# Optimization experiments

Measured on AMD Instinct MI355X. Metric: run time of the kernel, lower is better.

The kernel has to match this reference:

```python
import jax, jax.numpy as jnp
import numpy as np
from jax import lax

B, T, F = 8, 512, 128          # batch, mel time, mel freq
DM, DS, DC, EXP, NL = 384, 16, 4, 2, 12
DI = EXP * DM                   # 768 inner width
DTR = (DM + 15) // 16           # 24, mamba_ssm dt_rank='auto'
PT = PF = 16
L = (T // PT) * (F // PF)       # 256 patches
NC = 4


def setup_inputs() -> dict:
    key = jax.random.key(0)
    ks = iter(jax.random.split(key, 24))
    def n(shape, s=0.02):
        return jax.random.normal(next(ks), shape, jnp.float32) * s
    return {
        "x": jax.random.normal(next(ks), (B, T, F), jnp.float32),
        "patch_w": n((DM, PT, PF)),
        "patch_b": jnp.zeros((DM,), jnp.float32),
        "pos_embed": n((1, L, DM)),
        "ln_g": jnp.ones((NL, DM), jnp.float32),
        "ln_b": jnp.zeros((NL, DM), jnp.float32),
        "in_proj_w": n((NL, 2 * DI, DM)),
        "conv_w": n((NL, DI, DC), 0.1),
        "conv_b": jnp.zeros((NL, DI), jnp.float32),
        "x_proj_w": n((NL, DTR + 2 * DS, DI)),
        "dt_proj_w": n((NL, DI, DTR), 0.1),
        "dt_proj_b": n((NL, DI), 0.1),
        "A_log": jnp.tile(jnp.log(jnp.arange(1, DS + 1, dtype=jnp.float32))[None, None, :], (NL, DI, 1)),
        "Dskip": jnp.ones((NL, DI), jnp.float32),
        "out_proj_w": n((NL, DM, DI)),
        "fn_g": jnp.ones((DM,), jnp.float32),
        "fn_b": jnp.zeros((DM,), jnp.float32),
        "head_w": n((NC, DM)),
        "head_b": jnp.zeros((NC,), jnp.float32),
    }


def _layernorm(x, g, b):
    m = x.mean(-1, keepdims=True)
    v = jnp.var(x, axis=-1, keepdims=True)
    return (x - m) * lax.rsqrt(v + 1e-5) * g + b


def _silu(v):
    return v * jax.nn.sigmoid(v)


def _mamba_block(x, p):
    # x: [B, L, DM]; residual Mamba block (pre-LN, dropout=identity in eval)
    ln_g, ln_b, Wi, cw, cb, Wx, Wdt, bdt, A_log, Dsk, Wo = p
    res = x
    h = _layernorm(x, ln_g, ln_b)
    xz = jnp.einsum('bld,ed->ble', h, Wi)          # [B,L,2*DI]
    u, z = jnp.split(xz, 2, axis=-1)
    # causal depthwise conv1d, kernel DC (small, unrolled)
    up = jnp.pad(u, ((0, 0), (DC - 1, 0), (0, 0)))
    u = sum(up[:, k:k + L, :] * cw[:, k] for k in range(DC)) + cb
    u = _silu(u)
    proj = jnp.einsum('bld,ed->ble', u, Wx)        # [B,L,DTR+2*DS]
    dt, Bm, Cm = jnp.split(proj, [DTR, DTR + DS], axis=-1)
    delta = jax.nn.softplus(jnp.einsum('blr,dr->bld', dt, Wdt) + bdt)  # [B,L,DI]
    A = -jnp.exp(A_log)                            # [DI, DS]
    dA = jnp.exp(delta[..., None] * A)             # [B,L,DI,DS]
    dBu = (delta * u)[..., None] * Bm[:, :, None, :]

    def step(hst, inp):
        dA_t, dBu_t, C_t = inp
        hst = dA_t * hst + dBu_t                   # [B,DI,DS]
        return hst, jnp.einsum('bdn,bn->bd', hst, C_t)

    h0 = jnp.zeros((x.shape[0], DI, DS), x.dtype)
    _, ys = lax.scan(step, h0, (dA.swapaxes(0, 1), dBu.swapaxes(0, 1), Cm.swapaxes(0, 1)))
    y = ys.swapaxes(0, 1) + u * Dsk                # [B,L,DI]
    y = y * _silu(z)
    return res + jnp.einsum('bld,ed->ble', y, Wo)


def reference(x, patch_w, patch_b, pos_embed, ln_g, ln_b, in_proj_w, conv_w, conv_b,
              x_proj_w, dt_proj_w, dt_proj_b, A_log, Dskip, out_proj_w,
              fn_g, fn_b, head_w, head_b):
    Bn = x.shape[0]
    # patch embed = non-overlapping 16x16 conv == blocked reshape + einsum
    patches = x.reshape(Bn, T // PT, PT, F // PF, PF)
    tok = jnp.einsum('bhpwq,dpq->bhwd', patches, patch_w) + patch_b
    tok = tok.reshape(Bn, L, DM) + pos_embed

    def layer(carry, p):
        return _mamba_block(carry, p), None

    tok, _ = lax.scan(layer, tok, (ln_g, ln_b, in_proj_w, conv_w, conv_b,
                                   x_proj_w, dt_proj_w, dt_proj_b, A_log, Dskip, out_proj_w))
    tok = _layernorm(tok, fn_g, fn_b)
    pooled = tok.mean(axis=1)
    return pooled @ head_w.T + head_b
```

## Files before the change

### kernel.cpp

```cpp
#include <hip/hip_runtime.h>
#include <math.h>

namespace {

constexpr int kB   = 8;
constexpr int kL   = 256;
constexpr int kTok = 2048;
constexpr int kDM  = 384;
constexpr int kDI  = 768;
constexpr int kDS  = 16;
constexpr int kDTR = 24;
constexpr int kPROJ = 56;
constexpr int kNL  = 12;

constexpr int kWIN  = 2 * kDI * kDM;
constexpr int kWOUT = kDM * kDI;
constexpr int kWX   = kPROJ * kDI;
constexpr int kWTOT = kWIN + kWOUT + kWX;

typedef float f32x4 __attribute__((ext_vector_type(4)));
typedef short short8 __attribute__((ext_vector_type(8)));

__device__ __forceinline__ float softplus_f(float x) {
  return (x > 20.f) ? x : log1pf(__expf(x));
}
__device__ __forceinline__ float silu_f(float x) {
  return x / (1.f + __expf(-x));
}
__device__ __forceinline__ unsigned short f2bf(float f) {
  union { float f; unsigned u; } v; v.f = f;
  unsigned r = v.u + 0x7FFFu + ((v.u >> 16) & 1u);
  return (unsigned short)(r >> 16);
}
__device__ __forceinline__ float bf2f(unsigned short u) {
  return __uint_as_float((unsigned)u << 16);
}

__global__ __launch_bounds__(256) void patch_gemm_k(
    const float* __restrict__ x, const float* __restrict__ Bw,
    const float* __restrict__ bias, const float* __restrict__ pos,
    float* __restrict__ C) {
  __shared__ float As[16][68];
  __shared__ float Bs[16][68];
  int tid = threadIdx.x;
  int bm = blockIdx.y * 64;
  int bn = blockIdx.x * 64;
  int lr = tid >> 2;
  int lk = (tid & 3) << 2;
  int tm = (tid >> 4) << 2;
  int tn = (tid & 15) << 2;
  float acc[4][4] = {};
  for (int k0 = 0; k0 < 256; k0 += 16) {
    {
      int token = bm + lr;
      int b = token >> 8, l = token & 255;
      int h = l >> 3, w = l & 7;
      int p = k0 >> 4;
      const float* ap = x + ((size_t)(b * 512) + h * 16 + p) * 128 + w * 16 + lk;
      float4 av = *(const float4*)ap;
      As[lk + 0][lr] = av.x; As[lk + 1][lr] = av.y;
      As[lk + 2][lr] = av.z; As[lk + 3][lr] = av.w;
    }
    {
      const float* bp = Bw + (size_t)(bn + lr) * 256 + k0 + lk;
      float4 bv = *(const float4*)bp;
      Bs[lk + 0][lr] = bv.x; Bs[lk + 1][lr] = bv.y;
      Bs[lk + 2][lr] = bv.z; Bs[lk + 3][lr] = bv.w;
    }
    __syncthreads();
    #pragma unroll
    for (int k = 0; k < 16; ++k) {
      float4 a = *(const float4*)&As[k][tm];
      float4 b = *(const float4*)&Bs[k][tn];
      float av[4] = {a.x, a.y, a.z, a.w};
      float bv[4] = {b.x, b.y, b.z, b.w};
      #pragma unroll
      for (int i = 0; i < 4; ++i)
        #pragma unroll
        for (int j = 0; j < 4; ++j)
          acc[i][j] = fmaf(av[i], bv[j], acc[i][j]);
    }
    __syncthreads();
  }
  #pragma unroll
  for (int i = 0; i < 4; ++i) {
    int row = bm + tm + i;
    #pragma unroll
    for (int j = 0; j < 4; ++j) {
      int col = bn + tn + j;
      C[(size_t)row * kDM + col] =
          acc[i][j] + bias[col] + pos[(size_t)(row & 255) * kDM + col];
    }
  }
}

__global__ __launch_bounds__(384) void lnpool_k(
    const float* __restrict__ in, float* __restrict__ pooled,
    const float* __restrict__ g, const float* __restrict__ bb) {
  int t = blockIdx.x, d = threadIdx.x;
  float v = in[(size_t)t * kDM + d];
  float s = v, s2 = v * v;
  #pragma unroll
  for (int m = 32; m >= 1; m >>= 1) {
    s  += __shfl_xor(s, m);
    s2 += __shfl_xor(s2, m);
  }
  __shared__ float ps[6], ps2[6];
  if ((d & 63) == 0) { ps[d >> 6] = s; ps2[d >> 6] = s2; }
  __syncthreads();
  float S = 0.f, S2 = 0.f;
  #pragma unroll
  for (int i = 0; i < 6; ++i) { S += ps[i]; S2 += ps2[i]; }
  float mean = S * (1.f / 384.f);
  float var  = S2 * (1.f / 384.f) - mean * mean;
  float r = rsqrtf(var + 1e-5f);
  float o = (v - mean) * r * g[d] + bb[d];
  atomicAdd(&pooled[(size_t)(t >> 8) * kDM + d], o * (1.f / 256.f));
}

__global__ __launch_bounds__(256) void convert_all_k(
    const float* __restrict__ w_in, const float* __restrict__ w_out,
    const float* __restrict__ w_x, unsigned short* __restrict__ dst,
    float* __restrict__ pooled_zero) {
  int layer = blockIdx.y;
  int tid = threadIdx.x;
  if (layer == 0 && blockIdx.x == 0) {
    for (int i = tid; i < kB * kDM; i += 256) pooled_zero[i] = 0.f;
  }
  int i4 = (blockIdx.x * 256 + tid) * 4;
  if (i4 >= kWTOT) return;
  const float* src;
  int off;
  if (i4 < kWIN) { src = w_in + (size_t)layer * kWIN; off = i4; }
  else if (i4 < kWIN + kWOUT) { src = w_out + (size_t)layer * kWOUT; off = i4 - kWIN; }
  else { src = w_x + (size_t)layer * kWX; off = i4 - kWIN - kWOUT; }
  float4 v = *(const float4*)(src + off);
  unsigned short o[4] = {f2bf(v.x), f2bf(v.y), f2bf(v.z), f2bf(v.w)};
  *(uint2*)(dst + (size_t)layer * kWTOT + i4) = *(const uint2*)o;
}

__global__ __launch_bounds__(256) void inproj_ln_k(
    const float* __restrict__ tok, const unsigned short* __restrict__ Bw,
    const float* __restrict__ g, const float* __restrict__ bb,
    unsigned short* __restrict__ Cbf, float* __restrict__ proj_zero) {
  __shared__ __align__(16) unsigned short As[4][64][8];
  __shared__ __align__(16) unsigned short Bs[4][128][8];
  __shared__ float smean[64], srstd[64];
  __shared__ float sg_[kDM], sb_[kDM];
  int tid = threadIdx.x;
  int bm = blockIdx.y * 64;
  int bn = blockIdx.x * 128;
  {
    int bid = blockIdx.y * 12 + blockIdx.x;
    for (int i = bid * 256 + tid; i < kTok * kPROJ; i += 384 * 256)
      proj_zero[i] = 0.f;
  }
  for (int i = tid; i < kDM; i += 256) { sg_[i] = g[i]; sb_[i] = bb[i]; }
  {
    int r = tid >> 2, quarter = tid & 3;
    const float* rp = tok + (size_t)(bm + r) * kDM + quarter * 96;
    float s = 0.f, s2 = 0.f;
    #pragma unroll
    for (int q = 0; q < 24; ++q) {
      float4 v = ((const float4*)rp)[q];
      s  += v.x + v.y + v.z + v.w;
      s2 += v.x * v.x + v.y * v.y + v.z * v.z + v.w * v.w;
    }
    s  += __shfl_xor(s, 1);  s2 += __shfl_xor(s2, 1);
    s  += __shfl_xor(s, 2);  s2 += __shfl_xor(s2, 2);
    if (quarter == 0) {
      float mean = s * (1.f / 384.f);
      float var  = s2 * (1.f / 384.f) - mean * mean;
      smean[r] = mean;
      srstd[r] = rsqrtf(var + 1e-5f);
    }
  }
  __syncthreads();
  int wave = tid >> 6, lane = tid & 63;
  int lm = lane & 15, lq = lane >> 4;
  int wm = (wave & 1) * 32, wn = (wave >> 1) * 64;
  f32x4 acc[2][4] = {};
  for (int k0 = 0; k0 < kDM; k0 += 32) {
    int ar = tid & 63, aq = tid >> 6;
    unsigned short av[8];
    {
      float mean = smean[ar], rstd = srstd[ar];
      const float* ap = tok + (size_t)(bm + ar) * kDM + k0 + aq * 8;
      float4 v0 = ((const float4*)ap)[0];
      float4 v1 = ((const float4*)ap)[1];
      float vv[8] = {v0.x, v0.y, v0.z, v0.w, v1.x, v1.y, v1.z, v1.w};
      #pragma unroll
      for (int j = 0; j < 8; ++j) {
        int k = k0 + aq * 8 + j;
        av[j] = f2bf((vv[j] - mean) * rstd * sg_[k] + sb_[k]);
      }
    }
    int br = tid & 127, bq0 = tid >> 7, bq1 = bq0 + 2;
    uint4 b0 = *(const uint4*)(Bw + (size_t)(bn + br) * kDM + k0 + bq0 * 8);
    uint4 b1 = *(const uint4*)(Bw + (size_t)(bn + br) * kDM + k0 + bq1 * 8);
    __syncthreads();
    *(uint4*)&As[aq][ar][0]  = *(const uint4*)av;
    *(uint4*)&Bs[bq0][br][0] = b0;
    *(uint4*)&Bs[bq1][br][0] = b1;
    __syncthreads();
    short8 bfrag[4];
    #pragma unroll
    for (int ni = 0; ni < 4; ++ni)
      bfrag[ni] = *(const short8*)&Bs[lq][wn + ni * 16 + lm][0];
    #pragma unroll
    for (int mi = 0; mi < 2; ++mi) {
      short8 afrag = *(const short8*)&As[lq][wm + mi * 16 + lm][0];
      #pragma unroll
      for (int ni = 0; ni < 4; ++ni)
        acc[mi][ni] = __builtin_amdgcn_mfma_f32_16x16x32_bf16(
            afrag, bfrag[ni], acc[mi][ni], 0, 0, 0);
    }
  }
  #pragma unroll
  for (int mi = 0; mi < 2; ++mi) {
    #pragma unroll
    for (int ni = 0; ni < 4; ++ni) {
      int grow0 = bm + wm + mi * 16 + lq * 4;
      int gcol = bn + wn + ni * 16 + lm;
      #pragma unroll
      for (int r = 0; r < 4; ++r)
        Cbf[(size_t)(grow0 + r) * (2 * kDI) + gcol] = f2bf(acc[mi][ni][r]);
    }
  }
}

__global__ __launch_bounds__(256) void xproj_conv_k(
    const unsigned short* __restrict__ xz, const unsigned short* __restrict__ Bw,
    const float* __restrict__ cw, const float* __restrict__ cb,
    float* __restrict__ proj, unsigned short* __restrict__ uT_bf) {
  __shared__ __align__(16) unsigned short As[4][64][8];
  __shared__ __align__(16) unsigned short Bs[4][64][8];
  __shared__ float scw[128][4];
  __shared__ float scb[128];
  int tid = threadIdx.x;
  int bm = blockIdx.x * 64;
  int kbase = blockIdx.y * 128;
  int wave = tid >> 6, lane = tid & 63;
  int lm = lane & 15, lq = lane >> 4;
  int wm = wave * 16;
  f32x4 acc[4] = {};

  if (tid < 128) {
    *(float4*)&scw[tid][0] = *(const float4*)(cw + (size_t)(kbase + tid) * 4);
    scb[tid] = cb[kbase + tid];
  }
  __syncthreads();

  int ar = tid & 63;
  int aq = tid >> 6;
  int t = bm + ar;
  int b = t >> 8, l = t & 255;

  for (int kt = 0; kt < 4; ++kt) {
    int k0 = kbase + kt * 32;
    int dloc = kt * 32 + aq * 8;
    int dg = kbase + dloc;
    unsigned short av[8];
    {
      float vals[4][8];
      #pragma unroll
      for (int q = 0; q < 4; ++q) {
        if (l - 3 + q >= 0) {
          uint4 r = *(const uint4*)(xz + (size_t)(t - 3 + q) * (2 * kDI) + dg);
          const unsigned short* rs = (const unsigned short*)&r;
          #pragma unroll
          for (int j = 0; j < 8; ++j) vals[q][j] = bf2f(rs[j]);
        } else {
          #pragma unroll
          for (int j = 0; j < 8; ++j) vals[q][j] = 0.f;
        }
      }
      #pragma unroll
      for (int j = 0; j < 8; ++j) {
        float a = scb[dloc + j];
        a = fmaf(vals[0][j], scw[dloc + j][0], a);
        a = fmaf(vals[1][j], scw[dloc + j][1], a);
        a = fmaf(vals[2][j], scw[dloc + j][2], a);
        a = fmaf(vals[3][j], scw[dloc + j][3], a);
        unsigned short ub = f2bf(silu_f(a));
        av[j] = ub;
        uT_bf[((size_t)b * kDI + dg + j) * kL + l] = ub;
      }
    }
    int br = tid & 63, bq = tid >> 6;
    uint4 b0;
    if (br < kPROJ)
      b0 = *(const uint4*)(Bw + (size_t)br * kDI + k0 + bq * 8);
    else
      b0 = make_uint4(0u, 0u, 0u, 0u);
    __syncthreads();
    *(uint4*)&As[aq][ar][0] = *(const uint4*)av;
    *(uint4*)&Bs[bq][br][0] = b0;
    __syncthreads();
    short8 afrag = *(const short8*)&As[lq][wm + lm][0];
    #pragma unroll
    for (int ni = 0; ni < 4; ++ni) {
      short8 bfrag = *(const short8*)&Bs[lq][ni * 16 + lm][0];
      acc[ni] = __builtin_amdgcn_mfma_f32_16x16x32_bf16(
          afrag, bfrag, acc[ni], 0, 0, 0);
    }
  }

  #pragma unroll
  for (int ni = 0; ni < 4; ++ni) {
    int grow0 = bm + wm + lq * 4;
    int gcol = ni * 16 + lm;
    if (gcol < kPROJ) {
      #pragma unroll
      for (int r = 0; r < 4; ++r)
        atomicAdd(&proj[(size_t)(grow0 + r) * kPROJ + gcol], acc[ni][r]);
    }
  }
}

__global__ __launch_bounds__(256) void bgemm_out_k(
    const unsigned short* __restrict__ A, int lda,
    const unsigned short* __restrict__ B, int ldb,
    float* __restrict__ C, int ldc, int Kc) {
  __shared__ __align__(16) unsigned short As[4][128][8];
  __shared__ __align__(16) unsigned short Bs[4][128][8];
  int tid = threadIdx.x;
  int bm = blockIdx.y * 128;
  int bn = blockIdx.x * 128;
  int k_begin = blockIdx.z * Kc;
  int wave = tid >> 6, lane = tid & 63;
  int lm = lane & 15, lq = lane >> 4;
  int wm = (wave >> 1) * 64, wn = (wave & 1) * 64;
  f32x4 acc[4][4] = {};

  for (int kt = 0; kt < Kc; kt += 32) {
    int k0 = k_begin + kt;
    int ar0 = tid & 127, aq0 = tid >> 7;
    int aq1 = aq0 + 2;
    uint4 a0 = *(const uint4*)(A + (size_t)(bm + ar0) * lda + k0 + aq0 * 8);
    uint4 a1 = *(const uint4*)(A + (size_t)(bm + ar0) * lda + k0 + aq1 * 8);
    uint4 b0 = *(const uint4*)(B + (size_t)(bn + ar0) * ldb + k0 + aq0 * 8);
    uint4 b1 = *(const uint4*)(B + (size_t)(bn + ar0) * ldb + k0 + aq1 * 8);
    __syncthreads();
    *(uint4*)&As[aq0][ar0][0] = a0;
    *(uint4*)&As[aq1][ar0][0] = a1;
    *(uint4*)&Bs[aq0][ar0][0] = b0;
    *(uint4*)&Bs[aq1][ar0][0] = b1;
    __syncthreads();
    short8 bfrag[4];
    #pragma unroll
    for (int ni = 0; ni < 4; ++ni)
      bfrag[ni] = *(const short8*)&Bs[lq][wn + ni * 16 + lm][0];
    #pragma unroll
    for (int mi = 0; mi < 4; ++mi) {
      short8 afrag = *(const short8*)&As[lq][wm + mi * 16 + lm][0];
      #pragma unroll
      for (int ni = 0; ni < 4; ++ni)
        acc[mi][ni] = __builtin_amdgcn_mfma_f32_16x16x32_bf16(
            afrag, bfrag[ni], acc[mi][ni], 0, 0, 0);
    }
  }

  #pragma unroll
  for (int mi = 0; mi < 4; ++mi) {
    #pragma unroll
    for (int ni = 0; ni < 4; ++ni) {
      int grow0 = bm + wm + mi * 16 + lq * 4;
      int gcol = bn + wn + ni * 16 + lm;
      #pragma unroll
      for (int r = 0; r < 4; ++r)
        atomicAdd(&C[(size_t)(grow0 + r) * ldc + gcol], acc[mi][ni][r]);
    }
  }
}

__global__ __launch_bounds__(256) void scansplit_k(
    const float* __restrict__ proj, const unsigned short* __restrict__ uT_bf,
    const unsigned short* __restrict__ xz, const float* __restrict__ dtw,
    const float* __restrict__ dtb, const float* __restrict__ A_log,
    const float* __restrict__ Dsk, unsigned short* __restrict__ y_bf) {
  int d0 = blockIdx.x * 8;
  int b = blockIdx.y;
  int tid = threadIdx.x;
  int dsub = tid & 7;
  int nh = (tid >> 3) & 1;
  int c = tid >> 4;
  int d = d0 + dsub;
  __shared__ float sh[16][16][9];
  __shared__ float sca[16][16][9];

  float Av[8];
  {
    const float* ap = A_log + (size_t)d * kDS + nh * 8;
    #pragma unroll
    for (int q = 0; q < 2; ++q) {
      float4 v = ((const float4*)ap)[q];
      Av[q * 4 + 0] = -__expf(v.x);
      Av[q * 4 + 1] = -__expf(v.y);
      Av[q * 4 + 2] = -__expf(v.z);
      Av[q * 4 + 3] = -__expf(v.w);
    }
  }
  float bdt = dtb[d];
  float Dv = Dsk[d];

  const float* pr = proj + ((size_t)(b * kL) + c * 16) * kPROJ;

  float dtlo[8], dthi[8];
  {
    float wdt[24];
    const float* wp = dtw + (size_t)d * kDTR;
    #pragma unroll
    for (int q = 0; q < 6; ++q) {
      float4 v = ((const float4*)wp)[q];
      wdt[q * 4 + 0] = v.x; wdt[q * 4 + 1] = v.y;
      wdt[q * 4 + 2] = v.z; wdt[q * 4 + 3] = v.w;
    }
    const float* prm = pr + (size_t)(nh * 8) * kPROJ;
    float mine[8];
    #pragma unroll
    for (int i = 0; i < 8; ++i) {
      const float* p = prm + (size_t)i * kPROJ;
      float acc = bdt;
      #pragma unroll
      for (int q = 0; q < 6; ++q) {
        float4 v = ((const float4*)p)[q];
        acc = fmaf(v.x, wdt[q * 4 + 0], acc);
        acc = fmaf(v.y, wdt[q * 4 + 1], acc);
        acc = fmaf(v.z, wdt[q * 4 + 2], acc);
        acc = fmaf(v.w, wdt[q * 4 + 3], acc);
      }
      mine[i] = softplus_f(acc);
    }
    #pragma unroll
    for (int i = 0; i < 8; ++i) {
      float other = __shfl_xor(mine[i], 8);
      dtlo[i] = nh ? other : mine[i];
      dthi[i] = nh ? mine[i] : other;
    }
  }

  float u_[16];
  {
    const unsigned short* up = uT_bf + ((size_t)b * kDI + d) * kL + c * 16;
    uint4 v0 = ((const uint4*)up)[0];
    uint4 v1 = ((const uint4*)up)[1];
    const unsigned short* us = (const unsigned short*)&v0;
    #pragma unroll
    for (int i = 0; i < 8; ++i) u_[i] = bf2f(us[i]);
    us = (const unsigned short*)&v1;
    #pragma unroll
    for (int i = 0; i < 8; ++i) u_[8 + i] = bf2f(us[i]);
  }

  float h[8], ca[8];
  #pragma unroll
  for (int n = 0; n < 8; ++n) { h[n] = 0.f; ca[n] = 1.f; }
  #pragma unroll
  for (int i = 0; i < 16; ++i) {
    float dl = (i < 8) ? dtlo[i] : dthi[i - 8];
    float du = dl * u_[i];
    const float* p = pr + (size_t)i * kPROJ + 24 + nh * 8;
    float4 b0 = ((const float4*)p)[0];
    float4 b1 = ((const float4*)p)[1];
    float Bv[8] = {b0.x, b0.y, b0.z, b0.w, b1.x, b1.y, b1.z, b1.w};
    #pragma unroll
    for (int n = 0; n < 8; ++n) {
      float a = __expf(dl * Av[n]);
      h[n] = fmaf(a, h[n], du * Bv[n]);
      ca[n] *= a;
    }
  }
  {
    int nrow = nh * 8;
    #pragma unroll
    for (int q = 0; q < 8; ++q) {
      sh[c][nrow + q][dsub] = h[q];
      sca[c][nrow + q][dsub] = ca[q];
    }
  }
  __syncthreads();

  float h0[8];
  #pragma unroll
  for (int n = 0; n < 8; ++n) h0[n] = 0.f;
  {
    int nrow = nh * 8;
    for (int j = 0; j < c; ++j) {
      #pragma unroll
      for (int q = 0; q < 8; ++q)
        h0[q] = fmaf(sca[j][nrow + q][dsub], h0[q], sh[j][nrow + q][dsub]);
    }
  }

  float sg_[16];
  if (nh == 0) {
    const unsigned short* zp =
        xz + (size_t)(b * kL + c * 16) * (2 * kDI) + kDI + d;
    #pragma unroll
    for (int i = 0; i < 16; ++i)
      sg_[i] = silu_f(bf2f(zp[(size_t)i * (2 * kDI)]));
  }

  unsigned short* yp = y_bf + (size_t)(b * kL + c * 16) * kDI + d;
  #pragma unroll
  for (int i = 0; i < 16; ++i) {
    float dl = (i < 8) ? dtlo[i] : dthi[i - 8];
    float du = dl * u_[i];
    const float* p = pr + (size_t)i * kPROJ + 24 + nh * 8;
    float4 b0 = ((const float4*)p)[0];
    float4 b1 = ((const float4*)p)[1];
    float4 c0 = ((const float4*)(p + 16))[0];
    float4 c1 = ((const float4*)(p + 16))[1];
    float Bv[8] = {b0.x, b0.y, b0.z, b0.w, b1.x, b1.y, b1.z, b1.w};
    float Cv[8] = {c0.x, c0.y, c0.z, c0.w, c1.x, c1.y, c1.z, c1.w};
    float yv = 0.f;
    #pragma unroll
    for (int n = 0; n < 8; ++n) {
      float a = __expf(dl * Av[n]);
      h0[n] = fmaf(a, h0[n], du * Bv[n]);
      yv = fmaf(h0[n], Cv[n], yv);
    }
    yv += __shfl_xor(yv, 8);
    if (nh == 0) yp[(size_t)i * kDI] = f2bf((yv + u_[i] * Dv) * sg_[i]);
  }
}

__global__ __launch_bounds__(64) void head_k(
    const float* __restrict__ pooled, const float* __restrict__ hw,
    const float* __restrict__ hb, float* __restrict__ out) {
  int b = blockIdx.x >> 2, c = blockIdx.x & 3;
  int lane = threadIdx.x;
  float acc = 0.f;
  for (int dd = lane; dd < kDM; dd += 64)
    acc = fmaf(pooled[b * kDM + dd], hw[c * kDM + dd], acc);
  #pragma unroll
  for (int m = 32; m >= 1; m >>= 1) acc += __shfl_xor(acc, m);
  if (lane == 0) out[b * 4 + c] = acc + hb[c];
}

}

extern "C" void kernel_launch(void* const* d_in, const int* in_sizes, int n_in,
                              void* d_out, int out_size, void* d_ws, size_t ws_size,
                              hipStream_t stream) {
  (void)in_sizes; (void)n_in; (void)out_size; (void)ws_size;
  const float* x        = (const float*)d_in[0];
  const float* patch_w  = (const float*)d_in[1];
  const float* patch_b  = (const float*)d_in[2];
  const float* pos      = (const float*)d_in[3];
  const float* ln_g     = (const float*)d_in[4];
  const float* ln_b     = (const float*)d_in[5];
  const float* in_w     = (const float*)d_in[6];
  const float* conv_w   = (const float*)d_in[7];
  const float* conv_b   = (const float*)d_in[8];
  const float* xproj_w  = (const float*)d_in[9];
  const float* dtproj_w = (const float*)d_in[10];
  const float* dtproj_b = (const float*)d_in[11];
  const float* A_log    = (const float*)d_in[12];
  const float* Dskip    = (const float*)d_in[13];
  const float* out_w    = (const float*)d_in[14];
  const float* fn_g     = (const float*)d_in[15];
  const float* fn_b     = (const float*)d_in[16];
  const float* head_w   = (const float*)d_in[17];
  const float* head_b   = (const float*)d_in[18];
  float* out = (float*)d_out;

  float* ws = (float*)d_ws;
  float* tok    = ws; ws += kTok * kDM;
  float* proj   = ws; ws += kTok * kPROJ;
  float* pooled = ws; ws += kB * kDM;
  unsigned short* xz_bf = (unsigned short*)ws; ws += kTok * 2 * kDI / 2;
  unsigned short* uT_bf = (unsigned short*)ws; ws += kTok * kDI / 2;
  unsigned short* y_bf  = (unsigned short*)ws; ws += kTok * kDI / 2;
  unsigned short* w_bf  = (unsigned short*)ws; ws += (size_t)kNL * kWTOT / 2;

  convert_all_k<<<dim3(kWTOT / 4 / 256, kNL), 256, 0, stream>>>(
      in_w, out_w, xproj_w, w_bf, pooled);

  patch_gemm_k<<<dim3(6, 32), 256, 0, stream>>>(x, patch_w, patch_b, pos, tok);

  for (int layer = 0; layer < kNL; ++layer) {
    const unsigned short* wl = w_bf + (size_t)layer * kWTOT;
    inproj_ln_k<<<dim3(12, 32), 256, 0, stream>>>(
        tok, wl, ln_g + layer * kDM, ln_b + layer * kDM, xz_bf, proj);
    xproj_conv_k<<<dim3(32, 6), 256, 0, stream>>>(
        xz_bf, wl + kWIN + kWOUT, conv_w + layer * kDI * 4,
        conv_b + layer * kDI, proj, uT_bf);
    scansplit_k<<<dim3(kDI / 8, kB), 256, 0, stream>>>(
        proj, uT_bf, xz_bf, dtproj_w + (size_t)layer * kDI * kDTR,
        dtproj_b + layer * kDI, A_log + (size_t)layer * kDI * kDS,
        Dskip + layer * kDI, y_bf);
    bgemm_out_k<<<dim3(3, 16, 4), 256, 0, stream>>>(
        y_bf, kDI, wl + kWIN, kDI, tok, kDM, kDI / 4);
  }

  lnpool_k<<<kTok, kDM, 0, stream>>>(tok, pooled, fn_g, fn_b);
  head_k<<<kB * 4, 64, 0, stream>>>(pooled, head_w, head_b, out);
}
```

Baseline: 1.147 ms.

## Use linearity to skip second scan pass and halve chunk length in scan

The chunked selective scan now runs a single local pass per chunk. Each step records the chunk-local output and the cumulative-decay-weighted C coefficients, packed as bf16 in registers. The carried-in prefix state is then added through a dot product, so the exp-heavy recurrence is not recomputed a second time. Chunks shrink from 16 to 8 timesteps (32 chunks, 4 channels per block), which doubles the grid and halves per-thread sequential work. The cost is a longer serial cross-chunk prefix loop, more registers, and bf16 rounding of the correction coefficients, which can slightly change numerics.

```diff
diff --git a/kernel.cpp b/kernel.cpp
--- a/kernel.cpp
+++ b/kernel.cpp
@@ -374,20 +374,20 @@
   }
 }
 
-__global__ __launch_bounds__(256) void scansplit_k(
+__global__ __launch_bounds__(256) void scanfast_k(
     const float* __restrict__ proj, const unsigned short* __restrict__ uT_bf,
     const unsigned short* __restrict__ xz, const float* __restrict__ dtw,
     const float* __restrict__ dtb, const float* __restrict__ A_log,
     const float* __restrict__ Dsk, unsigned short* __restrict__ y_bf) {
-  int d0 = blockIdx.x * 8;
+  int d0 = blockIdx.x * 4;
   int b = blockIdx.y;
   int tid = threadIdx.x;
-  int dsub = tid & 7;
-  int nh = (tid >> 3) & 1;
-  int c = tid >> 4;
+  int dsub = tid & 3;
+  int nh = (tid >> 2) & 1;
+  int c = tid >> 3;
   int d = d0 + dsub;
-  __shared__ float sh[16][16][9];
-  __shared__ float sca[16][16][9];
+  __shared__ float sh[32][16][5];
+  __shared__ float sca[32][16][5];
 
   float Av[8];
   {
@@ -404,9 +404,9 @@
   float bdt = dtb[d];
   float Dv = Dsk[d];
 
-  const float* pr = proj + ((size_t)(b * kL) + c * 16) * kPROJ;
-
-  float dtlo[8], dthi[8];
+  const float* pr = proj + ((size_t)(b * kL) + c * 8) * kPROJ;
+
+  float dt_[8];
   {
     float wdt[24];
     const float* wp = dtw + (size_t)d * kDTR;
@@ -416,10 +416,10 @@
       wdt[q * 4 + 0] = v.x; wdt[q * 4 + 1] = v.y;
       wdt[q * 4 + 2] = v.z; wdt[q * 4 + 3] = v.w;
     }
-    const float* prm = pr + (size_t)(nh * 8) * kPROJ;
-    float mine[8];
-    #pragma unroll
-    for (int i = 0; i < 8; ++i) {
+    const float* prm = pr + (size_t)(nh * 4) * kPROJ;
+    float mine[4];
+    #pragma unroll
+    for (int i = 0; i < 4; ++i) {
       const float* p = prm + (size_t)i * kPROJ;
       float acc = bdt;
       #pragma unroll
@@ -433,79 +433,30 @@
       mine[i] = softplus_f(acc);
     }
     #pragma unroll
-    for (int i = 0; i < 8; ++i) {
-      float other = __shfl_xor(mine[i], 8);
-      dtlo[i] = nh ? other : mine[i];
-      dthi[i] = nh ? mine[i] : other;
-    }
-  }
-
-  float u_[16];
+    for (int i = 0; i < 4; ++i) {
+      float oth = __shfl_xor(mine[i], 4);
+      dt_[i]     = nh ? oth : mine[i];
+      dt_[4 + i] = nh ? mine[i] : oth;
+    }
+  }
+
+  float u_[8];
   {
-    const unsigned short* up = uT_bf + ((size_t)b * kDI + d) * kL + c * 16;
-    uint4 v0 = ((const uint4*)up)[0];
-    uint4 v1 = ((const uint4*)up)[1];
-    const unsigned short* us = (const unsigned short*)&v0;
+    const unsigned short* up = uT_bf + ((size_t)b * kDI + d) * kL + c * 8;
+    uint4 v = *(const uint4*)up;
+    const unsigned short* us = (const unsigned short*)&v;
     #pragma unroll
     for (int i = 0; i < 8; ++i) u_[i] = bf2f(us[i]);
-    us = (const unsigned short*)&v1;
-    #pragma unroll
-    for (int i = 0; i < 8; ++i) u_[8 + i] = bf2f(us[i]);
   }
 
   float h[8], ca[8];
   #pragma unroll
   for (int n = 0; n < 8; ++n) { h[n] = 0.f; ca[n] = 1.f; }
-  #pragma unroll
-  for (int i = 0; i < 16; ++i) {
-    float dl = (i < 8) ? dtlo[i] : dthi[i - 8];
-    float du = dl * u_[i];
-    const float* p = pr + (size_t)i * kPROJ + 24 + nh * 8;
-    float4 b0 = ((const float4*)p)[0];
-    float4 b1 = ((const float4*)p)[1];
-    float Bv[8] = {b0.x, b0.y, b0.z, b0.w, b1.x, b1.y, b1.z, b1.w};
-    #pragma unroll
-    for (int n = 0; n < 8; ++n) {
-      float a = __expf(dl * Av[n]);
-      h[n] = fmaf(a, h[n], du * Bv[n]);
-      ca[n] *= a;
-    }
-  }
-  {
-    int nrow = nh * 8;
-    #pragma unroll
-    for (int q = 0; q < 8; ++q) {
-      sh[c][nrow + q][dsub] = h[q];
-      sca[c][nrow + q][dsub] = ca[q];
-    }
-  }
-  __syncthreads();
-
-  float h0[8];
-  #pragma unroll
-  for (int n = 0; n < 8; ++n) h0[n] = 0.f;
-  {
-    int nrow = nh * 8;
-    for (int j = 0; j < c; ++j) {
-      #pragma unroll
-      for (int q = 0; q < 8; ++q)
-        h0[q] = fmaf(sca[j][nrow + q][dsub], h0[q], sh[j][nrow + q][dsub]);
-    }
-  }
-
-  float sg_[16];
-  if (nh == 0) {
-    const unsigned short* zp =
-        xz + (size_t)(b * kL + c * 16) * (2 * kDI) + kDI + d;
-    #pragma unroll
-    for (int i = 0; i < 16; ++i)
-      sg_[i] = silu_f(bf2f(zp[(size_t)i * (2 * kDI)]));
-  }
-
-  unsigned short* yp = y_bf + (size_t)(b * kL + c * 16) * kDI + d;
-  #pragma unroll
-  for (int i = 0; i < 16; ++i) {
-    float dl = (i < 8) ? dtlo[i] : dthi[i - 8];
+  float s_[8];
+  unsigned cg[8][4];
+  #pragma unroll
+  for (int i = 0; i < 8; ++i) {
+    float dl = dt_[i];
     float du = dl * u_[i];
     const float* p = pr + (size_t)i * kPROJ + 24 + nh * 8;
     float4 b0 = ((const float4*)p)[0];
@@ -514,14 +465,64 @@
     float4 c1 = ((const float4*)(p + 16))[1];
     float Bv[8] = {b0.x, b0.y, b0.z, b0.w, b1.x, b1.y, b1.z, b1.w};
     float Cv[8] = {c0.x, c0.y, c0.z, c0.w, c1.x, c1.y, c1.z, c1.w};
-    float yv = 0.f;
+    float sv = 0.f;
     #pragma unroll
     for (int n = 0; n < 8; ++n) {
       float a = __expf(dl * Av[n]);
-      h0[n] = fmaf(a, h0[n], du * Bv[n]);
-      yv = fmaf(h0[n], Cv[n], yv);
-    }
-    yv += __shfl_xor(yv, 8);
+      h[n] = fmaf(a, h[n], du * Bv[n]);
+      ca[n] *= a;
+      sv = fmaf(h[n], Cv[n], sv);
+    }
+    s_[i] = sv;
+    #pragma unroll
+    for (int q = 0; q < 4; ++q) {
+      unsigned lo = f2bf(Cv[q * 2] * ca[q * 2]);
+      unsigned hi = f2bf(Cv[q * 2 + 1] * ca[q * 2 + 1]);
+      cg[i][q] = lo | (hi << 16);
+    }
+  }
+  {
+    int nrow = nh * 8;
+    #pragma unroll
+    for (int q = 0; q < 8; ++q) {
+      sh[c][nrow + q][dsub] = h[q];
+      sca[c][nrow + q][dsub] = ca[q];
+    }
+  }
+  __syncthreads();
+
+  float h0[8];
+  #pragma unroll
+  for (int n = 0; n < 8; ++n) h0[n] = 0.f;
+  {
+    int nrow = nh * 8;
+    for (int j = 0; j < c; ++j) {
+      #pragma unroll
+      for (int q = 0; q < 8; ++q)
+        h0[q] = fmaf(sca[j][nrow + q][dsub], h0[q], sh[j][nrow + q][dsub]);
+    }
+  }
+
+  float sg_[8];
+  if (nh == 0) {
+    const unsigned short* zp =
+        xz + (size_t)(b * kL + c * 8) * (2 * kDI) + kDI + d;
+    #pragma unroll
+    for (int i = 0; i < 8; ++i)
+      sg_[i] = silu_f(bf2f(zp[(size_t)i * (2 * kDI)]));
+  }
+
+  unsigned short* yp = y_bf + (size_t)(b * kL + c * 8) * kDI + d;
+  #pragma unroll
+  for (int i = 0; i < 8; ++i) {
+    float yv = s_[i];
+    #pragma unroll
+    for (int q = 0; q < 4; ++q) {
+      unsigned pk = cg[i][q];
+      yv = fmaf(bf2f((unsigned short)(pk & 0xFFFFu)), h0[q * 2], yv);
+      yv = fmaf(bf2f((unsigned short)(pk >> 16)), h0[q * 2 + 1], yv);
+    }
+    yv += __shfl_xor(yv, 4);
     if (nh == 0) yp[(size_t)i * kDI] = f2bf((yv + u_[i] * Dv) * sg_[i]);
   }
 }
@@ -587,7 +588,7 @@
     xproj_conv_k<<<dim3(32, 6), 256, 0, stream>>>(
         xz_bf, wl + kWIN + kWOUT, conv_w + layer * kDI * 4,
         conv_b + layer * kDI, proj, uT_bf);
-    scansplit_k<<<dim3(kDI / 8, kB), 256, 0, stream>>>(
+    scanfast_k<<<dim3(kDI / 4, kB), 256, 0, stream>>>(
         proj, uT_bf, xz_bf, dtproj_w + (size_t)layer * kDI * kDTR,
         dtproj_b + layer * kDI, A_log + (size_t)layer * kDI * kDS,
         Dskip + layer * kDI, y_bf);
```

New measurement: 1.166 ms. About the same (+1.7%).
